# Performance work log

Measured on AMD Instinct MI355X. Metric: run time of the kernel, lower is better.

## Reference

```python
import jax, jax.numpy as jnp
import numpy as np

B, L, SIZE, ATT, LIN = 8, 2048, 1024, 1024, 4096
EPS = 1e-5


def layer_norm(x, g, b):
    m = x.mean(-1, keepdims=True)
    v = ((x - m) ** 2).mean(-1, keepdims=True)
    return (x - m) * jax.lax.rsqrt(v + EPS) * g + b


def time_shift(x):
    # ZeroPad2d((0,0,1,-1)): prepend a zero timestep, drop the last one
    return jnp.pad(x, ((0, 0), (1, 0), (0, 0)))[:, :-1]


def wkv(time_decay, time_first, k, v):
    """RWKV-v4 WKV linear-attention recurrence (numerically stable, log-space max tracking).
    k, v: (B, L, D). Returns (B, L, D)."""
    w = -jnp.exp(time_decay)  # (D,) per-channel decay (negative)
    u = time_first            # (D,) bonus for current token

    def step(carry, kv):
        p, q, o = carry  # numerator, denominator, running max exponent: (B, D)
        kt, vt = kv      # (B, D)
        no = jnp.maximum(o, u + kt)
        A = jnp.exp(o - no)
        Bc = jnp.exp(u + kt - no)
        out = (A * p + Bc * vt) / (A * q + Bc)
        no2 = jnp.maximum(o + w, kt)
        A2 = jnp.exp(o + w - no2)
        B2 = jnp.exp(kt - no2)
        return (A2 * p + B2 * vt, A2 * q + B2, no2), out

    Bn, Ln, D = k.shape
    init = (jnp.zeros((Bn, D), k.dtype), jnp.zeros((Bn, D), k.dtype),
            jnp.full((Bn, D), -1e38, k.dtype))
    _, out = jax.lax.scan(step, init, (jnp.moveaxis(k, 1, 0), jnp.moveaxis(v, 1, 0)))
    return jnp.moveaxis(out, 0, 1)


def setup_inputs() -> dict:
    key = jax.random.key(0)
    ks = jax.random.split(key, 20)
    n = lambda i, shape, s=1.0: jax.random.normal(ks[i], shape, jnp.float32) * s
    u = lambda i, shape: jax.random.uniform(ks[i], shape, jnp.float32)
    return {
        "x": n(0, (B, L, SIZE)),
        "ln_att_g": jnp.ones((SIZE,), jnp.float32), "ln_att_b": jnp.zeros((SIZE,), jnp.float32),
        "ln_ffn_g": jnp.ones((SIZE,), jnp.float32), "ln_ffn_b": jnp.zeros((SIZE,), jnp.float32),
        "att_time_decay": n(1, (ATT,), 0.5), "att_time_first": n(2, (ATT,), 0.5),
        "att_mix_k": u(3, (SIZE,)), "att_mix_v": u(4, (SIZE,)), "att_mix_r": u(5, (SIZE,)),
        "att_wk": n(6, (SIZE, ATT), 0.02), "att_wv": n(7, (SIZE, ATT), 0.02),
        "att_wr": n(8, (SIZE, ATT), 0.02), "att_wo": n(9, (ATT, SIZE), 0.02),
        "ffn_mix_k": u(10, (SIZE,)), "ffn_mix_r": u(11, (SIZE,)),
        "ffn_wk": n(12, (SIZE, LIN), 0.02), "ffn_wv": n(13, (LIN, SIZE), 0.02),
        "ffn_wr": n(14, (SIZE, SIZE), 0.02),
    }


def reference(x, ln_att_g, ln_att_b, ln_ffn_g, ln_ffn_b,
              att_time_decay, att_time_first, att_mix_k, att_mix_v, att_mix_r,
              att_wk, att_wv, att_wr, att_wo,
              ffn_mix_k, ffn_mix_r, ffn_wk, ffn_wv, ffn_wr):
    # --- time-mixing (WKV attention) branch ---
    h = layer_norm(x, ln_att_g, ln_att_b)
    sx = time_shift(h)
    k = (h * att_mix_k + sx * (1.0 - att_mix_k)) @ att_wk
    v = (h * att_mix_v + sx * (1.0 - att_mix_v)) @ att_wv
    r = jax.nn.sigmoid((h * att_mix_r + sx * (1.0 - att_mix_r)) @ att_wr)
    att = (r * wkv(att_time_decay, att_time_first, k, v)) @ att_wo
    x = x + att  # dropout rate 0.0 (eval)
    # --- channel-mixing (FFN) branch ---
    h = layer_norm(x, ln_ffn_g, ln_ffn_b)
    sx = time_shift(h)
    kf = jnp.square(jax.nn.relu((h * ffn_mix_k + sx * (1.0 - ffn_mix_k)) @ ffn_wk))
    rf = jax.nn.sigmoid((h * ffn_mix_r + sx * (1.0 - ffn_mix_r)) @ ffn_wr)
    return x + rf * (kf @ ffn_wv)
```

## Files before the change

### kernel.cpp

```cpp
#include <hip/hip_runtime.h>
#include <cstdint>
#include <cstddef>

#define BB   8
#define LLEN 2048
#define DSZ  1024
#define FFN  4096
#define MROWS (BB*LLEN)
#define EPSLN 1e-5f
#define WKV_C 64
#define WKV_S (LLEN/WKV_C)
#define WKV_STATES (BB*WKV_C*DSZ)

typedef __bf16 bh8 __attribute__((ext_vector_type(8)));
typedef float  f32x4 __attribute__((ext_vector_type(4)));

__device__ __forceinline__ unsigned short f32_to_bf16(float f) {
  unsigned int u = __float_as_uint(f);
  u += 0x7FFFu + ((u >> 16) & 1u);
  return (unsigned short)(u >> 16);
}
__device__ __forceinline__ float bf16_to_f32(unsigned short u) {
  return __uint_as_float(((unsigned int)u) << 16);
}
__device__ __forceinline__ float bf16_lo(unsigned int u) {
  return __uint_as_float(u << 16);
}
__device__ __forceinline__ float bf16_hi(unsigned int u) {
  return __uint_as_float(u & 0xFFFF0000u);
}
__device__ __forceinline__ unsigned int pack_bf16(float lo, float hi) {
  return (unsigned int)f32_to_bf16(lo) | ((unsigned int)f32_to_bf16(hi) << 16);
}
__device__ __forceinline__ float fexp(float x) { return __expf(x); }
__device__ __forceinline__ float frcp(float x) { return __builtin_amdgcn_rcpf(x); }

__device__ __forceinline__ void load_lds16(const void* g, void* l) {
  __builtin_amdgcn_global_load_lds((const __attribute__((address_space(1))) void*)g,
                                   (__attribute__((address_space(3))) void*)l, 16, 0, 0);
}

#define RAW_BAR() asm volatile("s_barrier" ::: "memory")
#define WAIT_VM6() asm volatile("s_waitcnt vmcnt(6)" ::: "memory")
#define WAIT_VM0() asm volatile("s_waitcnt vmcnt(0)" ::: "memory")

struct TD { const float* s; unsigned short* d; int K; int N; };
struct TDs { TD t[7]; int base[8]; };

__global__ __launch_bounds__(256) void transpose_all(TDs td) {
  __shared__ float tile[32][33];
  int bid = blockIdx.x;
  int i = 0;
#pragma unroll
  for (int j = 1; j < 7; ++j) if (bid >= td.base[j]) i = j;
  const float* W = td.t[i].s;
  unsigned short* Wt = td.t[i].d;
  int K = td.t[i].K, N = td.t[i].N;
  int lid = bid - td.base[i];
  int gx = N >> 5;
  int n0 = (lid % gx) * 32, k0 = (lid / gx) * 32;
  int tx = threadIdx.x & 31, ty = threadIdx.x >> 5;
#pragma unroll
  for (int j = 0; j < 32; j += 8)
    tile[ty + j][tx] = W[(size_t)(k0 + ty + j) * N + n0 + tx];
  __syncthreads();
#pragma unroll
  for (int j = 0; j < 32; j += 8)
    Wt[(size_t)(n0 + ty + j) * K + k0 + tx] = f32_to_bf16(tile[tx][ty + j]);
}

__global__ __launch_bounds__(256) void lnmix_att(const float* __restrict__ x,
                                                 const float* __restrict__ g,
                                                 const float* __restrict__ bb,
                                                 const float* __restrict__ mk,
                                                 const float* __restrict__ mv,
                                                 const float* __restrict__ mr,
                                                 unsigned short* __restrict__ xk,
                                                 unsigned short* __restrict__ xv,
                                                 unsigned short* __restrict__ xr) {
  int row = blockIdx.x;
  int t = row & (LLEN - 1);
  int tid = threadIdx.x;
  float4 vc = ((const float4*)(x + (size_t)row * DSZ))[tid];
  float4 vp = make_float4(0.f, 0.f, 0.f, 0.f);
  if (t > 0) vp = ((const float4*)(x + (size_t)(row - 1) * DSZ))[tid];
  float sc = vc.x + vc.y + vc.z + vc.w;
  float qc = vc.x * vc.x + vc.y * vc.y + vc.z * vc.z + vc.w * vc.w;
  float sp = vp.x + vp.y + vp.z + vp.w;
  float qp = vp.x * vp.x + vp.y * vp.y + vp.z * vp.z + vp.w * vp.w;
#pragma unroll
  for (int off = 32; off; off >>= 1) {
    sc += __shfl_down(sc, off); qc += __shfl_down(qc, off);
    sp += __shfl_down(sp, off); qp += __shfl_down(qp, off);
  }
  __shared__ float red[16];
  int lane = tid & 63, w = tid >> 6;
  if (lane == 0) { red[w] = sc; red[4 + w] = qc; red[8 + w] = sp; red[12 + w] = qp; }
  __syncthreads();
  if (tid < 4) red[tid * 4] = red[tid * 4] + red[tid * 4 + 1] + red[tid * 4 + 2] + red[tid * 4 + 3];
  __syncthreads();
  const float invD = 1.f / DSZ;
  float mc = red[0] * invD, rc = rsqrtf(red[4] * invD - mc * mc + EPSLN);
  float mp = red[8] * invD, rp = rsqrtf(red[12] * invD - mp * mp + EPSLN);
  float4 G = ((const float4*)g)[tid], Bv = ((const float4*)bb)[tid];
  float c[4] = { vc.x, vc.y, vc.z, vc.w };
  float p[4] = { vp.x, vp.y, vp.z, vp.w };
  float Ga[4] = { G.x, G.y, G.z, G.w };
  float Ba[4] = { Bv.x, Bv.y, Bv.z, Bv.w };
  float4 K = ((const float4*)mk)[tid];
  float4 V = ((const float4*)mv)[tid];
  float4 R = ((const float4*)mr)[tid];
  float Ka[4] = { K.x, K.y, K.z, K.w };
  float Va[4] = { V.x, V.y, V.z, V.w };
  float Ra[4] = { R.x, R.y, R.z, R.w };
  ushort4 ok, ov, orr;
  unsigned short* okp = &ok.x; unsigned short* ovp = &ov.x; unsigned short* orp = &orr.x;
#pragma unroll
  for (int e = 0; e < 4; ++e) {
    float hc = (c[e] - mc) * rc * Ga[e] + Ba[e];
    float hp = (t > 0) ? (p[e] - mp) * rp * Ga[e] + Ba[e] : 0.f;
    okp[e] = f32_to_bf16(hc * Ka[e] + hp * (1.f - Ka[e]));
    ovp[e] = f32_to_bf16(hc * Va[e] + hp * (1.f - Va[e]));
    orp[e] = f32_to_bf16(hc * Ra[e] + hp * (1.f - Ra[e]));
  }
  size_t e4 = (size_t)row * DSZ + tid * 4;
  *(ushort4*)(xk + e4) = ok;
  *(ushort4*)(xv + e4) = ov;
  *(ushort4*)(xr + e4) = orr;
}

__global__ __launch_bounds__(256) void lnmix_ffn(const float* __restrict__ x,
                                                 const float* __restrict__ g,
                                                 const float* __restrict__ bb,
                                                 const float* __restrict__ mk,
                                                 const float* __restrict__ mr,
                                                 unsigned short* __restrict__ xk,
                                                 unsigned short* __restrict__ xr) {
  int row = blockIdx.x;
  int t = row & (LLEN - 1);
  int tid = threadIdx.x;
  float4 vc = ((const float4*)(x + (size_t)row * DSZ))[tid];
  float4 vp = make_float4(0.f, 0.f, 0.f, 0.f);
  if (t > 0) vp = ((const float4*)(x + (size_t)(row - 1) * DSZ))[tid];
  float sc = vc.x + vc.y + vc.z + vc.w;
  float qc = vc.x * vc.x + vc.y * vc.y + vc.z * vc.z + vc.w * vc.w;
  float sp = vp.x + vp.y + vp.z + vp.w;
  float qp = vp.x * vp.x + vp.y * vp.y + vp.z * vp.z + vp.w * vp.w;
#pragma unroll
  for (int off = 32; off; off >>= 1) {
    sc += __shfl_down(sc, off); qc += __shfl_down(qc, off);
    sp += __shfl_down(sp, off); qp += __shfl_down(qp, off);
  }
  __shared__ float red[16];
  int lane = tid & 63, w = tid >> 6;
  if (lane == 0) { red[w] = sc; red[4 + w] = qc; red[8 + w] = sp; red[12 + w] = qp; }
  __syncthreads();
  if (tid < 4) red[tid * 4] = red[tid * 4] + red[tid * 4 + 1] + red[tid * 4 + 2] + red[tid * 4 + 3];
  __syncthreads();
  const float invD = 1.f / DSZ;
  float mc = red[0] * invD, rc = rsqrtf(red[4] * invD - mc * mc + EPSLN);
  float mp = red[8] * invD, rp = rsqrtf(red[12] * invD - mp * mp + EPSLN);
  float4 G = ((const float4*)g)[tid], Bv = ((const float4*)bb)[tid];
  float c[4] = { vc.x, vc.y, vc.z, vc.w };
  float p[4] = { vp.x, vp.y, vp.z, vp.w };
  float Ga[4] = { G.x, G.y, G.z, G.w };
  float Ba[4] = { Bv.x, Bv.y, Bv.z, Bv.w };
  float4 K = ((const float4*)mk)[tid];
  float4 R = ((const float4*)mr)[tid];
  float Ka[4] = { K.x, K.y, K.z, K.w };
  float Ra[4] = { R.x, R.y, R.z, R.w };
  ushort4 ok, orr;
  unsigned short* okp = &ok.x; unsigned short* orp = &orr.x;
#pragma unroll
  for (int e = 0; e < 4; ++e) {
    float hc = (c[e] - mc) * rc * Ga[e] + Ba[e];
    float hp = (t > 0) ? (p[e] - mp) * rp * Ga[e] + Ba[e] : 0.f;
    okp[e] = f32_to_bf16(hc * Ka[e] + hp * (1.f - Ka[e]));
    orp[e] = f32_to_bf16(hc * Ra[e] + hp * (1.f - Ra[e]));
  }
  size_t e4 = (size_t)row * DSZ + tid * 4;
  *(ushort4*)(xk + e4) = ok;
  *(ushort4*)(xr + e4) = orr;
}

__global__ __launch_bounds__(256) void wkv_pass1(const unsigned int* __restrict__ kk2,
                                                 const unsigned int* __restrict__ vv2,
                                                 const float* __restrict__ td,
                                                 float* __restrict__ sP,
                                                 float* __restrict__ sQ,
                                                 float* __restrict__ sO) {
  int gid = blockIdx.x * 256 + threadIdx.x;
  int d2 = gid & 511;
  int bc = gid >> 9;
  int c  = bc & (WKV_C - 1);
  int b  = bc >> 6;
  int d0 = d2 * 2;
  float w0 = -fexp(td[d0]), w1 = -fexp(td[d0 + 1]);
  size_t base = ((size_t)b * LLEN + (size_t)c * WKV_S) * 512 + d2;
  float p0 = 0.f, q0 = 0.f, o0 = -1e38f;
  float p1 = 0.f, q1 = 0.f, o1 = -1e38f;
  unsigned int kc = kk2[base], vc = vv2[base];
  unsigned int kA = 0, vA = 0, kB = 0, vB = 0;
  if (WKV_S > 1) { kA = kk2[base + 512]; vA = vv2[base + 512]; }
  for (int t = 0; t < WKV_S; ++t) {
    if (t + 2 < WKV_S) {
      size_t nxt = base + (size_t)(t + 2) * 512;
      kB = kk2[nxt]; vB = vv2[nxt];
    } else { kB = 0; vB = 0; }
    {
      float kt = bf16_lo(kc), vt = bf16_lo(vc);
      float ow = o0 + w0;
      float no2 = fmaxf(ow, kt);
      float A2 = fexp(ow - no2), B2 = fexp(kt - no2);
      p0 = A2 * p0 + B2 * vt; q0 = A2 * q0 + B2; o0 = no2;
    }
    {
      float kt = bf16_hi(kc), vt = bf16_hi(vc);
      float ow = o1 + w1;
      float no2 = fmaxf(ow, kt);
      float A2 = fexp(ow - no2), B2 = fexp(kt - no2);
      p1 = A2 * p1 + B2 * vt; q1 = A2 * q1 + B2; o1 = no2;
    }
    kc = kA; vc = vA; kA = kB; vA = vB;
  }
  int sidx = (bc << 10) + d0;
  sP[sidx] = p0; sP[sidx + 1] = p1;
  sQ[sidx] = q0; sQ[sidx + 1] = q1;
  sO[sidx] = o0; sO[sidx + 1] = o1;
}

__global__ __launch_bounds__(256) void wkv_combine(const float* __restrict__ sP,
                                                   const float* __restrict__ sQ,
                                                   const float* __restrict__ sO,
                                                   const float* __restrict__ td,
                                                   float* __restrict__ pP,
                                                   float* __restrict__ pQ,
                                                   float* __restrict__ pO) {
  int gid = blockIdx.x * 256 + threadIdx.x;
  int d = gid & (DSZ - 1);
  int b = gid >> 10;
  float w = -fexp(td[d]);
  float Sw = (float)WKV_S * w;
  float p = 0.f, q = 0.f, o = -1e38f;
  for (int c = 0; c < WKV_C; ++c) {
    size_t idx = (((size_t)b * WKV_C + c) << 10) + d;
    pP[idx] = p; pQ[idx] = q; pO[idx] = o;
    float lp = sP[idx], lq = sQ[idx], lo = sO[idx];
    float oin = o + Sw;
    float no  = fmaxf(oin, lo);
    float Ai  = fexp(oin - no);
    float Al  = fexp(lo - no);
    p = Ai * p + Al * lp;
    q = Ai * q + Al * lq;
    o = no;
  }
}

__global__ __launch_bounds__(256) void wkv_pass3(const unsigned int* __restrict__ kk2,
                                                 const unsigned int* __restrict__ vv2,
                                                 const unsigned int* __restrict__ rr2,
                                                 const float* __restrict__ td,
                                                 const float* __restrict__ tf,
                                                 const float* __restrict__ pP,
                                                 const float* __restrict__ pQ,
                                                 const float* __restrict__ pO,
                                                 unsigned int* __restrict__ rw2) {
  int gid = blockIdx.x * 256 + threadIdx.x;
  int d2 = gid & 511;
  int bc = gid >> 9;
  int c  = bc & (WKV_C - 1);
  int b  = bc >> 6;
  int d0 = d2 * 2;
  float w0 = -fexp(td[d0]), w1 = -fexp(td[d0 + 1]);
  float u0 = tf[d0], u1 = tf[d0 + 1];
  int sidx = (bc << 10) + d0;
  float p0 = pP[sidx], q0 = pQ[sidx], o0 = pO[sidx];
  float p1 = pP[sidx + 1], q1 = pQ[sidx + 1], o1 = pO[sidx + 1];
  size_t base = ((size_t)b * LLEN + (size_t)c * WKV_S) * 512 + d2;
  unsigned int kc = kk2[base], vc = vv2[base], rc = rr2[base];
  unsigned int kA = 0, vA = 0, rA = 0, kB = 0, vB = 0, rB = 0;
  if (WKV_S > 1) { kA = kk2[base + 512]; vA = vv2[base + 512]; rA = rr2[base + 512]; }
  for (int t = 0; t < WKV_S; ++t) {
    if (t + 2 < WKV_S) {
      size_t nxt = base + (size_t)(t + 2) * 512;
      kB = kk2[nxt]; vB = vv2[nxt]; rB = rr2[nxt];
    } else { kB = 0; vB = 0; rB = 0; }
    float out0, out1;
    {
      float kt = bf16_lo(kc), vt = bf16_lo(vc);
      float uk = u0 + kt;
      float no = fmaxf(o0, uk);
      float A  = fexp(o0 - no), Bc = fexp(uk - no);
      out0 = (A * p0 + Bc * vt) * frcp(A * q0 + Bc);
      float ow = o0 + w0;
      float no2 = fmaxf(ow, kt);
      float A2 = fexp(ow - no2), B2 = fexp(kt - no2);
      p0 = A2 * p0 + B2 * vt; q0 = A2 * q0 + B2; o0 = no2;
    }
    {
      float kt = bf16_hi(kc), vt = bf16_hi(vc);
      float uk = u1 + kt;
      float no = fmaxf(o1, uk);
      float A  = fexp(o1 - no), Bc = fexp(uk - no);
      out1 = (A * p1 + Bc * vt) * frcp(A * q1 + Bc);
      float ow = o1 + w1;
      float no2 = fmaxf(ow, kt);
      float A2 = fexp(ow - no2), B2 = fexp(kt - no2);
      p1 = A2 * p1 + B2 * vt; q1 = A2 * q1 + B2; o1 = no2;
    }
    rw2[base + (size_t)t * 512] = pack_bf16(bf16_lo(rc) * out0, bf16_hi(rc) * out1);
    kc = kA; vc = vA; rc = rA; kA = kB; vA = vB; rA = rB;
  }
}

#define KTILE(T, BUF, BUFN, KO1, KO2)                                             \
  {                                                                               \
    _Pragma("unroll")                                                             \
    for (int mi = 0; mi < 4; ++mi) {                                              \
      a03[mi][0] = *(const bh8*)(smA + (BUF) + aRow + mi * 2048 + sw0);           \
      a03[mi][1] = *(const bh8*)(smA + (BUF) + aRow + mi * 2048 + sw1);           \
    }                                                                             \
    _Pragma("unroll")                                                             \
    for (int nj = 0; nj < 2; ++nj) {                                              \
      b01[nj][0] = *(const bh8*)(smB + (BUF) + bRow + nj * 2048 + sw0);           \
      b01[nj][1] = *(const bh8*)(smB + (BUF) + bRow + nj * 2048 + sw1);           \
    }                                                                             \
    if ((T) + 1 < nk) {                                                           \
      load_lds16(pB1  + (KO1), smB + (BUFN) + 16384 + ldsW);                      \
      load_lds16(pB1b + (KO1), smB + (BUFN) + 16384 + 1024 + ldsW);               \
    }                                                                             \
    RAW_BAR();                                                                    \
    __builtin_amdgcn_s_setprio(1);                                                \
    _Pragma("unroll")                                                             \
    for (int mi = 0; mi < 4; ++mi)                                                \
      _Pragma("unroll")                                                           \
      for (int nj = 0; nj < 2; ++nj) {                                            \
        acc[mi][nj] = __builtin_amdgcn_mfma_f32_16x16x32_bf16(a03[mi][0], b01[nj][0], acc[mi][nj], 0, 0, 0); \
        acc[mi][nj] = __builtin_amdgcn_mfma_f32_16x16x32_bf16(a03[mi][1], b01[nj][1], acc[mi][nj], 0, 0, 0); \
      }                                                                           \
    __builtin_amdgcn_s_setprio(0);                                                \
    RAW_BAR();                                                                    \
    _Pragma("unroll")                                                             \
    for (int nj = 0; nj < 2; ++nj) {                                              \
      b23[nj][0] = *(const bh8*)(smB + (BUF) + bRow + (nj + 2) * 2048 + sw0);     \
      b23[nj][1] = *(const bh8*)(smB + (BUF) + bRow + (nj + 2) * 2048 + sw1);     \
    }                                                                             \
    RAW_BAR();                                                                    \
    __builtin_amdgcn_s_setprio(1);                                                \
    _Pragma("unroll")                                                             \
    for (int mi = 0; mi < 4; ++mi)                                                \
      _Pragma("unroll")                                                           \
      for (int nj = 0; nj < 2; ++nj) {                                            \
        acc[mi][nj + 2] = __builtin_amdgcn_mfma_f32_16x16x32_bf16(a03[mi][0], b23[nj][0], acc[mi][nj + 2], 0, 0, 0); \
        acc[mi][nj + 2] = __builtin_amdgcn_mfma_f32_16x16x32_bf16(a03[mi][1], b23[nj][1], acc[mi][nj + 2], 0, 0, 0); \
      }                                                                           \
    __builtin_amdgcn_s_setprio(0);                                                \
    RAW_BAR();                                                                    \
    _Pragma("unroll")                                                             \
    for (int mi = 0; mi < 4; ++mi) {                                              \
      a47[mi][0] = *(const bh8*)(smA + (BUF) + aRow + (mi + 4) * 2048 + sw0);     \
      a47[mi][1] = *(const bh8*)(smA + (BUF) + aRow + (mi + 4) * 2048 + sw1);     \
    }                                                                             \
    if ((T) + 2 < nk) {                                                           \
      load_lds16(pB0  + (KO2), smB + (BUF) + ldsW);                               \
      load_lds16(pB0b + (KO2), smB + (BUF) + 1024 + ldsW);                        \
    }                                                                             \
    RAW_BAR();                                                                    \
    __builtin_amdgcn_s_setprio(1);                                                \
    _Pragma("unroll")                                                             \
    for (int mi = 0; mi < 4; ++mi)                                                \
      _Pragma("unroll")                                                           \
      for (int nj = 0; nj < 2; ++nj) {                                            \
        acc[mi + 4][nj] = __builtin_amdgcn_mfma_f32_16x16x32_bf16(a47[mi][0], b01[nj][0], acc[mi + 4][nj], 0, 0, 0); \
        acc[mi + 4][nj] = __builtin_amdgcn_mfma_f32_16x16x32_bf16(a47[mi][1], b01[nj][1], acc[mi + 4][nj], 0, 0, 0); \
      }                                                                           \
    __builtin_amdgcn_s_setprio(0);                                                \
    RAW_BAR();                                                                    \
    if ((T) + 2 < nk) {                                                           \
      load_lds16(pA0  + (KO2), smA + (BUF) + ldsW);                               \
      load_lds16(pA0b + (KO2), smA + (BUF) + 1024 + ldsW);                        \
      load_lds16(pA1  + (KO2), smA + (BUF) + 16384 + ldsW);                       \
      load_lds16(pA1b + (KO2), smA + (BUF) + 16384 + 1024 + ldsW);                \
    }                                                                             \
    RAW_BAR();                                                                    \
    __builtin_amdgcn_s_setprio(1);                                                \
    _Pragma("unroll")                                                             \
    for (int mi = 0; mi < 4; ++mi)                                                \
      _Pragma("unroll")                                                           \
      for (int nj = 0; nj < 2; ++nj) {                                            \
        acc[mi + 4][nj + 2] = __builtin_amdgcn_mfma_f32_16x16x32_bf16(a47[mi][0], b23[nj][0], acc[mi + 4][nj + 2], 0, 0, 0); \
        acc[mi + 4][nj + 2] = __builtin_amdgcn_mfma_f32_16x16x32_bf16(a47[mi][1], b23[nj][1], acc[mi + 4][nj + 2], 0, 0, 0); \
      }                                                                           \
    __builtin_amdgcn_s_setprio(0);                                                \
    if ((T) + 2 < nk) { WAIT_VM6(); } else { WAIT_VM0(); }                        \
    RAW_BAR();                                                                    \
  }

#define GEMM_SETUP(AB, BB_, KD)                                                   \
  const unsigned short* Ab = (AB);                                                \
  const unsigned short* Bb = (BB_);                                               \
  const int nk = (KD) >> 6;                                                       \
  const int r15 = lane & 15;                                                      \
  const int sw0 = ((((lane >> 4)    ) ^ (lane & 7)) << 4);                        \
  const int sw1 = (((4 | (lane >> 4)) ^ (lane & 7)) << 4);                        \
  const int aRow = wr * 16384 + r15 * 128;                                        \
  const int bRow = wc * 8192  + r15 * 128;                                        \
  const int ldsW = wid * 2048 + lane * 16;                                        \
  const int grow = lane >> 3;                                                     \
  const int colS = (((lane & 7) ^ grow) << 3);                                    \
  const unsigned short* pA0  = Ab + (size_t)(wid * 16 + grow) * (KD) + colS;      \
  const unsigned short* pA0b = pA0 + (size_t)8 * (KD);                            \
  const unsigned short* pA1  = pA0 + (size_t)128 * (KD);                          \
  const unsigned short* pA1b = pA1 + (size_t)8 * (KD);                            \
  const unsigned short* pB0  = Bb + (size_t)(wid * 16 + grow) * (KD) + colS;      \
  const unsigned short* pB0b = pB0 + (size_t)8 * (KD);                            \
  const unsigned short* pB1  = pB0 + (size_t)128 * (KD);                          \
  const unsigned short* pB1b = pB1 + (size_t)8 * (KD);                            \
  f32x4 acc[8][4];                                                                \
  _Pragma("unroll")                                                               \
  for (int i = 0; i < 8; ++i)                                                     \
    _Pragma("unroll")                                                             \
    for (int j = 0; j < 4; ++j)                                                   \
      _Pragma("unroll")                                                           \
      for (int e = 0; e < 4; ++e) acc[i][j][e] = 0.f;                             \
  load_lds16(pA0,       smA + ldsW);                                              \
  load_lds16(pA0b,      smA + 1024 + ldsW);                                       \
  load_lds16(pA1,       smA + 16384 + ldsW);                                      \
  load_lds16(pA1b,      smA + 16384 + 1024 + ldsW);                               \
  load_lds16(pB0,       smB + ldsW);                                              \
  load_lds16(pB0b,      smB + 1024 + ldsW);                                       \
  load_lds16(pB1,       smB + 16384 + ldsW);                                      \
  load_lds16(pB1b,      smB + 16384 + 1024 + ldsW);                               \
  load_lds16(pB0 + 64,  smB + 32768 + ldsW);                                      \
  load_lds16(pB0b + 64, smB + 32768 + 1024 + ldsW);                               \
  load_lds16(pA0 + 64,  smA + 32768 + ldsW);                                      \
  load_lds16(pA0b + 64, smA + 32768 + 1024 + ldsW);                               \
  load_lds16(pA1 + 64,  smA + 32768 + 16384 + ldsW);                              \
  load_lds16(pA1b + 64, smA + 32768 + 16384 + 1024 + ldsW);                       \
  WAIT_VM6();                                                                     \
  RAW_BAR();                                                                      \
  bh8 a03[4][2], a47[4][2], b01[2][2], b23[2][2];                                 \
  for (int tb = 0; tb < nk; tb += 2) {                                            \
    KTILE(tb,     0,     32768, 64,  128);                                        \
    KTILE(tb + 1, 32768, 0,     128, 192);                                        \
    pA0 += 128; pA0b += 128; pA1 += 128; pA1b += 128;                             \
    pB0 += 128; pB0b += 128; pB1 += 128; pB1b += 128;                             \
  }

template <int EPI>
__global__ __launch_bounds__(512, 2) void gemm256(const unsigned short* __restrict__ A,
                                                  const unsigned short* __restrict__ Bt,
                                                  float* __restrict__ C,
                                                  unsigned short* __restrict__ Cbf,
                                                  const float* __restrict__ aux1,
                                                  const unsigned short* __restrict__ aux2b,
                                                  int M, int N, int K) {
  extern __shared__ unsigned char sm[];
  unsigned char* smA = sm;
  unsigned char* smB = sm + 65536;
  const int tid  = threadIdx.x;
  const int lane = tid & 63;
  const int wid  = tid >> 6;
  const int wr   = wid >> 2;
  const int wc   = wid & 3;
  int nwg = gridDim.x;
  int gx  = N >> 8;
  int wg  = blockIdx.x;
  int swzid = ((nwg & 7) == 0) ? ((wg & 7) * (nwg >> 3) + (wg >> 3)) : wg;
  int bn = swzid % gx, bm = swzid / gx;

  GEMM_SETUP(A + (size_t)bm * 256 * K, Bt + (size_t)bn * 256 * K, K)

  const int r4 = (lane >> 4) * 4, cn = lane & 15;
#pragma unroll
  for (int mi = 0; mi < 8; ++mi) {
#pragma unroll
    for (int nj = 0; nj < 4; ++nj) {
      int col = bn * 256 + wc * 64 + nj * 16 + cn;
#pragma unroll
      for (int e = 0; e < 4; ++e) {
        int row = bm * 256 + wr * 128 + mi * 16 + r4 + e;
        size_t idx = (size_t)row * N + col;
        float val = acc[mi][nj][e];
        if (EPI == 0) {
          Cbf[idx] = f32_to_bf16(val);
        } else if (EPI == 1) {
          Cbf[idx] = f32_to_bf16(frcp(1.f + fexp(-val)));
        } else if (EPI == 2) {
          C[idx] = aux1[idx] + val;
        } else if (EPI == 3) {
          float tt = val > 0.f ? val : 0.f;
          Cbf[idx] = f32_to_bf16(tt * tt);
        } else {
          C[idx] = aux1[idx] + bf16_to_f32(aux2b[idx]) * val;
        }
      }
    }
  }
}

__global__ __launch_bounds__(512, 2) void gemm256_kvr(const unsigned short* __restrict__ A0,
                                                      const unsigned short* __restrict__ A1,
                                                      const unsigned short* __restrict__ A2,
                                                      const unsigned short* __restrict__ B0w,
                                                      const unsigned short* __restrict__ B1w,
                                                      const unsigned short* __restrict__ B2w,
                                                      unsigned short* __restrict__ D0,
                                                      unsigned short* __restrict__ D1,
                                                      unsigned short* __restrict__ D2) {
  extern __shared__ unsigned char sm[];
  unsigned char* smA = sm;
  unsigned char* smB = sm + 65536;
  const int tid  = threadIdx.x;
  const int lane = tid & 63;
  const int wid  = tid >> 6;
  const int wr   = wid >> 2;
  const int wc   = wid & 3;
  int nwg = gridDim.x;
  int wg  = blockIdx.x;
  int swzid = (wg & 7) * (nwg >> 3) + (wg >> 3);
  int gsel  = swzid >> 8;
  int local = swzid & 255;
  int bn = local & 3, bm = local >> 2;

  const unsigned short* Asel = (gsel == 0) ? A0 : (gsel == 1) ? A1 : A2;
  const unsigned short* Bsel = (gsel == 0) ? B0w : (gsel == 1) ? B1w : B2w;
  unsigned short*       Dsel = (gsel == 0) ? D0 : (gsel == 1) ? D1 : D2;

  GEMM_SETUP(Asel + (size_t)bm * 256 * DSZ, Bsel + (size_t)bn * 256 * DSZ, DSZ)

  const int r4 = (lane >> 4) * 4, cn = lane & 15;
  const bool sig = (gsel == 2);
#pragma unroll
  for (int mi = 0; mi < 8; ++mi) {
#pragma unroll
    for (int nj = 0; nj < 4; ++nj) {
      int col = bn * 256 + wc * 64 + nj * 16 + cn;
#pragma unroll
      for (int e = 0; e < 4; ++e) {
        int row = bm * 256 + wr * 128 + mi * 16 + r4 + e;
        size_t idx = (size_t)row * DSZ + col;
        float val = acc[mi][nj][e];
        Dsel[idx] = f32_to_bf16(sig ? frcp(1.f + fexp(-val)) : val);
      }
    }
  }
}

extern "C" void kernel_launch(void* const* d_in, const int* in_sizes, int n_in,
                              void* d_out, int out_size, void* d_ws, size_t ws_size,
                              hipStream_t stream) {
  const float* x        = (const float*)d_in[0];
  const float* ln_att_g = (const float*)d_in[1];
  const float* ln_att_b = (const float*)d_in[2];
  const float* ln_ffn_g = (const float*)d_in[3];
  const float* ln_ffn_b = (const float*)d_in[4];
  const float* td       = (const float*)d_in[5];
  const float* tf       = (const float*)d_in[6];
  const float* amk      = (const float*)d_in[7];
  const float* amv      = (const float*)d_in[8];
  const float* amr      = (const float*)d_in[9];
  const float* att_wk   = (const float*)d_in[10];
  const float* att_wv   = (const float*)d_in[11];
  const float* att_wr   = (const float*)d_in[12];
  const float* att_wo   = (const float*)d_in[13];
  const float* fmk      = (const float*)d_in[14];
  const float* fmr      = (const float*)d_in[15];
  const float* ffn_wk   = (const float*)d_in[16];
  const float* ffn_wv   = (const float*)d_in[17];
  const float* ffn_wr   = (const float*)d_in[18];
  float* out = (float*)d_out;
  (void)in_sizes; (void)n_in; (void)out_size;

  const size_t WBYTES  = 4 * ((size_t)DSZ * DSZ * 2)
                       + (size_t)FFN * DSZ * 2
                       + (size_t)DSZ * FFN * 2
                       + (size_t)DSZ * DSZ * 2;
  const size_t BUF     = (size_t)MROWS * DSZ * 2;
  const size_t NEEDED  = WBYTES + 4 * BUF + 2 * BUF;
  if (ws_size < NEEDED) return;

  char* ws = (char*)d_ws;
  size_t off = 0;
  auto take = [&](size_t bytes) { char* p = ws + off; off += (bytes + 255) & ~(size_t)255; return p; };

  unsigned short* wkT  = (unsigned short*)take((size_t)DSZ * DSZ * 2);
  unsigned short* wvT  = (unsigned short*)take((size_t)DSZ * DSZ * 2);
  unsigned short* wrT  = (unsigned short*)take((size_t)DSZ * DSZ * 2);
  unsigned short* woT  = (unsigned short*)take((size_t)DSZ * DSZ * 2);
  unsigned short* fwkT = (unsigned short*)take((size_t)FFN * DSZ * 2);
  unsigned short* fwvT = (unsigned short*)take((size_t)DSZ * FFN * 2);
  unsigned short* fwrT = (unsigned short*)take((size_t)DSZ * DSZ * 2);
  unsigned short* bufA = (unsigned short*)take(BUF);
  unsigned short* bufB = (unsigned short*)take(BUF);
  unsigned short* bufC = (unsigned short*)take(BUF);
  unsigned short* bufD = (unsigned short*)take(BUF);
  char*           eReg = take(2 * BUF);
  unsigned short* kf = bufC;
  unsigned short* vBuf = (unsigned short*)eReg;
  unsigned short* rBuf = (unsigned short*)(eReg + BUF);

  float* sP = (float*)bufA;
  float* sQ = sP + WKV_STATES;
  float* sO = sQ + WKV_STATES;
  float* pP = sO + WKV_STATES;
  float* pQ = pP + WKV_STATES;
  float* pO = pQ + WKV_STATES;

  TDs tds;
  tds.t[0] = { att_wk, wkT,  DSZ, DSZ };
  tds.t[1] = { att_wv, wvT,  DSZ, DSZ };
  tds.t[2] = { att_wr, wrT,  DSZ, DSZ };
  tds.t[3] = { att_wo, woT,  DSZ, DSZ };
  tds.t[4] = { ffn_wr, fwrT, DSZ, DSZ };
  tds.t[5] = { ffn_wk, fwkT, DSZ, FFN };
  tds.t[6] = { ffn_wv, fwvT, FFN, DSZ };
  int acc = 0;
  for (int i = 0; i < 7; ++i) {
    tds.base[i] = acc;
    acc += (tds.t[i].N >> 5) * (tds.t[i].K >> 5);
  }
  tds.base[7] = acc;
  transpose_all<<<acc, 256, 0, stream>>>(tds);

  const int LDSB = 131072;
  const int G1   = (MROWS / 256) * (DSZ / 256);
  const int G2   = (MROWS / 256) * (FFN / 256);

  lnmix_att<<<MROWS, 256, 0, stream>>>(x, ln_att_g, ln_att_b, amk, amv, amr, bufA, bufB, bufC);
  gemm256_kvr<<<3 * G1, 512, LDSB, stream>>>(bufA, bufB, bufC, wkT, wvT, wrT, bufD, vBuf, rBuf);
  wkv_pass1<<<(WKV_STATES / 2) / 256, 256, 0, stream>>>((const unsigned int*)bufD, (const unsigned int*)vBuf, td, sP, sQ, sO);
  wkv_combine<<<(BB * DSZ) / 256, 256, 0, stream>>>(sP, sQ, sO, td, pP, pQ, pO);
  wkv_pass3<<<(WKV_STATES / 2) / 256, 256, 0, stream>>>((const unsigned int*)bufD, (const unsigned int*)vBuf, (const unsigned int*)rBuf, td, tf, pP, pQ, pO, (unsigned int*)bufB);
  gemm256<2><<<G1, 512, LDSB, stream>>>(bufB, woT, out, nullptr, x, nullptr, MROWS, DSZ, DSZ);

  lnmix_ffn<<<MROWS, 256, 0, stream>>>(out, ln_ffn_g, ln_ffn_b, fmk, fmr, bufA, bufB);
  gemm256<3><<<G2, 512, LDSB, stream>>>(bufA, fwkT, nullptr, kf, nullptr, nullptr, MROWS, FFN, DSZ);
  gemm256<1><<<G1, 512, LDSB, stream>>>(bufB, fwrT, nullptr, bufA, nullptr, nullptr, MROWS, DSZ, DSZ);
  gemm256<4><<<G1, 512, LDSB, stream>>>(kf, fwvT, out, nullptr, out, bufA, MROWS, DSZ, FFN);
}
```

Baseline: 630.2 us.

## Restructure GEMM k-loop prefetch schedule and remove intermediate barriers

```diff
diff --git a/kernel.cpp b/kernel.cpp
--- a/kernel.cpp
+++ b/kernel.cpp
@@ -41,7 +41,7 @@
 }
 
 #define RAW_BAR() asm volatile("s_barrier" ::: "memory")
-#define WAIT_VM6() asm volatile("s_waitcnt vmcnt(6)" ::: "memory")
+#define WAIT_VM4() asm volatile("s_waitcnt vmcnt(4)" ::: "memory")
 #define WAIT_VM0() asm volatile("s_waitcnt vmcnt(0)" ::: "memory")
 
 struct TD { const float* s; unsigned short* d; int K; int N; };
@@ -313,23 +313,33 @@
   }
 }
 
-#define KTILE(T, BUF, BUFN, KO1, KO2)                                             \
+#define KTILE_BODY(T)                                                             \
   {                                                                               \
+    const int buf  = ((T) & 1) << 15;                                             \
+    const int bufn = buf ^ 32768;                                                 \
+    bh8 a03[4][2], a47[4][2], b01[2][2], b23[2][2];                               \
+                                                           \
     _Pragma("unroll")                                                             \
     for (int mi = 0; mi < 4; ++mi) {                                              \
-      a03[mi][0] = *(const bh8*)(smA + (BUF) + aRow + mi * 2048 + sw0);           \
-      a03[mi][1] = *(const bh8*)(smA + (BUF) + aRow + mi * 2048 + sw1);           \
+      a03[mi][0] = *(const bh8*)(smA + buf + aRow + mi * 2048 + sw0);             \
+      a03[mi][1] = *(const bh8*)(smA + buf + aRow + mi * 2048 + sw1);             \
     }                                                                             \
     _Pragma("unroll")                                                             \
     for (int nj = 0; nj < 2; ++nj) {                                              \
-      b01[nj][0] = *(const bh8*)(smB + (BUF) + bRow + nj * 2048 + sw0);           \
-      b01[nj][1] = *(const bh8*)(smB + (BUF) + bRow + nj * 2048 + sw1);           \
+      b01[nj][0] = *(const bh8*)(smB + buf + bRow + nj * 2048 + sw0);             \
+      b01[nj][1] = *(const bh8*)(smB + buf + bRow + nj * 2048 + sw1);             \
+    }                                                                             \
+    _Pragma("unroll")                                                             \
+    for (int nj = 0; nj < 2; ++nj) {                                              \
+      b23[nj][0] = *(const bh8*)(smB + buf + bRow + (nj + 2) * 2048 + sw0);       \
+      b23[nj][1] = *(const bh8*)(smB + buf + bRow + (nj + 2) * 2048 + sw1);       \
     }                                                                             \
     if ((T) + 1 < nk) {                                                           \
-      load_lds16(pB1  + (KO1), smB + (BUFN) + 16384 + ldsW);                      \
-      load_lds16(pB1b + (KO1), smB + (BUFN) + 16384 + 1024 + ldsW);               \
+      load_lds16(pA0  + 64, smA + bufn + ldsW);                                   \
+      load_lds16(pA0b + 64, smA + bufn + 1024 + ldsW);                            \
+      load_lds16(pA1  + 64, smA + bufn + 16384 + ldsW);                           \
+      load_lds16(pA1b + 64, smA + bufn + 16384 + 1024 + ldsW);                    \
     }                                                                             \
-    RAW_BAR();                                                                    \
     __builtin_amdgcn_s_setprio(1);                                                \
     _Pragma("unroll")                                                             \
     for (int mi = 0; mi < 4; ++mi)                                                \
@@ -338,15 +348,6 @@
         acc[mi][nj] = __builtin_amdgcn_mfma_f32_16x16x32_bf16(a03[mi][0], b01[nj][0], acc[mi][nj], 0, 0, 0); \
         acc[mi][nj] = __builtin_amdgcn_mfma_f32_16x16x32_bf16(a03[mi][1], b01[nj][1], acc[mi][nj], 0, 0, 0); \
       }                                                                           \
-    __builtin_amdgcn_s_setprio(0);                                                \
-    RAW_BAR();                                                                    \
-    _Pragma("unroll")                                                             \
-    for (int nj = 0; nj < 2; ++nj) {                                              \
-      b23[nj][0] = *(const bh8*)(smB + (BUF) + bRow + (nj + 2) * 2048 + sw0);     \
-      b23[nj][1] = *(const bh8*)(smB + (BUF) + bRow + (nj + 2) * 2048 + sw1);     \
-    }                                                                             \
-    RAW_BAR();                                                                    \
-    __builtin_amdgcn_s_setprio(1);                                                \
     _Pragma("unroll")                                                             \
     for (int mi = 0; mi < 4; ++mi)                                                \
       _Pragma("unroll")                                                           \
@@ -356,16 +357,18 @@
       }                                                                           \
     __builtin_amdgcn_s_setprio(0);                                                \
     RAW_BAR();                                                                    \
+                                                           \
     _Pragma("unroll")                                                             \
     for (int mi = 0; mi < 4; ++mi) {                                              \
-      a47[mi][0] = *(const bh8*)(smA + (BUF) + aRow + (mi + 4) * 2048 + sw0);     \
-      a47[mi][1] = *(const bh8*)(smA + (BUF) + aRow + (mi + 4) * 2048 + sw1);     \
+      a47[mi][0] = *(const bh8*)(smA + buf + aRow + (mi + 4) * 2048 + sw0);       \
+      a47[mi][1] = *(const bh8*)(smA + buf + aRow + (mi + 4) * 2048 + sw1);       \
     }                                                                             \
     if ((T) + 2 < nk) {                                                           \
-      load_lds16(pB0  + (KO2), smB + (BUF) + ldsW);                               \
-      load_lds16(pB0b + (KO2), smB + (BUF) + 1024 + ldsW);                        \
+      load_lds16(pB0  + 128, smB + buf + ldsW);                                   \
+      load_lds16(pB0b + 128, smB + buf + 1024 + ldsW);                            \
+      load_lds16(pB1  + 128, smB + buf + 16384 + ldsW);                           \
+      load_lds16(pB1b + 128, smB + buf + 16384 + 1024 + ldsW);                    \
     }                                                                             \
-    RAW_BAR();                                                                    \
     __builtin_amdgcn_s_setprio(1);                                                \
     _Pragma("unroll")                                                             \
     for (int mi = 0; mi < 4; ++mi)                                                \
@@ -374,16 +377,6 @@
         acc[mi + 4][nj] = __builtin_amdgcn_mfma_f32_16x16x32_bf16(a47[mi][0], b01[nj][0], acc[mi + 4][nj], 0, 0, 0); \
         acc[mi + 4][nj] = __builtin_amdgcn_mfma_f32_16x16x32_bf16(a47[mi][1], b01[nj][1], acc[mi + 4][nj], 0, 0, 0); \
       }                                                                           \
-    __builtin_amdgcn_s_setprio(0);                                                \
-    RAW_BAR();                                                                    \
-    if ((T) + 2 < nk) {                                                           \
-      load_lds16(pA0  + (KO2), smA + (BUF) + ldsW);                               \
-      load_lds16(pA0b + (KO2), smA + (BUF) + 1024 + ldsW);                        \
-      load_lds16(pA1  + (KO2), smA + (BUF) + 16384 + ldsW);                       \
-      load_lds16(pA1b + (KO2), smA + (BUF) + 16384 + 1024 + ldsW);                \
-    }                                                                             \
-    RAW_BAR();                                                                    \
-    __builtin_amdgcn_s_setprio(1);                                                \
     _Pragma("unroll")                                                             \
     for (int mi = 0; mi < 4; ++mi)                                                \
       _Pragma("unroll")                                                           \
@@ -392,7 +385,7 @@
         acc[mi + 4][nj + 2] = __builtin_amdgcn_mfma_f32_16x16x32_bf16(a47[mi][1], b23[nj][1], acc[mi + 4][nj + 2], 0, 0, 0); \
       }                                                                           \
     __builtin_amdgcn_s_setprio(0);                                                \
-    if ((T) + 2 < nk) { WAIT_VM6(); } else { WAIT_VM0(); }                        \
+    if ((T) + 2 < nk) { WAIT_VM4(); } else { WAIT_VM0(); }                        \
     RAW_BAR();                                                                    \
   }
 
@@ -423,6 +416,7 @@
     for (int j = 0; j < 4; ++j)                                                   \
       _Pragma("unroll")                                                           \
       for (int e = 0; e < 4; ++e) acc[i][j][e] = 0.f;                             \
+        \
   load_lds16(pA0,       smA + ldsW);                                              \
   load_lds16(pA0b,      smA + 1024 + ldsW);                                       \
   load_lds16(pA1,       smA + 16384 + ldsW);                                      \
@@ -431,20 +425,20 @@
   load_lds16(pB0b,      smB + 1024 + ldsW);                                       \
   load_lds16(pB1,       smB + 16384 + ldsW);                                      \
   load_lds16(pB1b,      smB + 16384 + 1024 + ldsW);                               \
-  load_lds16(pB0 + 64,  smB + 32768 + ldsW);                                      \
-  load_lds16(pB0b + 64, smB + 32768 + 1024 + ldsW);                               \
-  load_lds16(pA0 + 64,  smA + 32768 + ldsW);                                      \
-  load_lds16(pA0b + 64, smA + 32768 + 1024 + ldsW);                               \
-  load_lds16(pA1 + 64,  smA + 32768 + 16384 + ldsW);                              \
-  load_lds16(pA1b + 64, smA + 32768 + 16384 + 1024 + ldsW);                       \
-  WAIT_VM6();                                                                     \
+  if (nk > 1) {                                                                   \
+    load_lds16(pB0  + 64, smB + 32768 + ldsW);                                    \
+    load_lds16(pB0b + 64, smB + 32768 + 1024 + ldsW);                             \
+    load_lds16(pB1  + 64, smB + 32768 + 16384 + ldsW);                            \
+    load_lds16(pB1b + 64, smB + 32768 + 16384 + 1024 + ldsW);                     \
+    WAIT_VM4();                                                                   \
+  } else {                                                                        \
+    WAIT_VM0();                                                                   \
+  }                                                                               \
   RAW_BAR();                                                                      \
-  bh8 a03[4][2], a47[4][2], b01[2][2], b23[2][2];                                 \
-  for (int tb = 0; tb < nk; tb += 2) {                                            \
-    KTILE(tb,     0,     32768, 64,  128);                                        \
-    KTILE(tb + 1, 32768, 0,     128, 192);                                        \
-    pA0 += 128; pA0b += 128; pA1 += 128; pA1b += 128;                             \
-    pB0 += 128; pB0b += 128; pB1 += 128; pB1b += 128;                             \
+  for (int tb = 0; tb < nk; ++tb) {                                               \
+    KTILE_BODY(tb)                                                                \
+    pA0 += 64; pA0b += 64; pA1 += 64; pA1b += 64;                                 \
+    pB0 += 64; pB0b += 64; pB1 += 64; pB1b += 64;                                 \
   }
 
 template <int EPI>
```

Result: faster. 613.0 us (-2.7%).
